# Kernel tuning notes

Measured on AMD Instinct MI355X. Metric: run time of the kernel, lower is better.

## Reference

```python
import jax, jax.numpy as jnp
import numpy as np

B, NV, H, D = 8, 16, 192, 512
NH = 8
HD = D // NH
DFF = 2048
EPS = 1e-5


def _bn(x, g, b):
    # x: (N, T, C); BatchNorm1d over channel C using batch stats (train mode)
    mu = jnp.mean(x, axis=(0, 1))
    var = jnp.var(x, axis=(0, 1))
    return (x - mu) / jnp.sqrt(var + EPS) * g + b


def _ff(x, w1, b1, w2, b2):
    h = jax.nn.gelu(jnp.einsum('bnhd,fd->bnhf', x, w1) + b1, approximate=False)
    return jnp.einsum('bnhf,df->bnhd', h, w2) + b2


def setup_inputs() -> dict:
    key = jax.random.key(0)
    ks = jax.random.split(key, 20)
    s = 0.02
    return {
        'src': jax.random.normal(ks[0], (B, NV, H, D), jnp.float32),
        'qk_w': jax.random.normal(ks[1], (2 * D, D), jnp.float32) * s,
        'qk_b': jnp.zeros((2 * D,), jnp.float32),
        'v_w': jax.random.normal(ks[2], (D, D), jnp.float32) * s,
        'v_b': jnp.zeros((D,), jnp.float32),
        'alpha_p': jax.random.normal(ks[3], (HD, 1), jnp.float32) * 0.1,
        'g_pre1': jnp.ones((D,), jnp.float32),
        'b_pre1': jnp.zeros((D,), jnp.float32),
        'g_pre2': jnp.ones((D,), jnp.float32),
        'b_pre2': jnp.zeros((D,), jnp.float32),
        'ff1_w1': jax.random.normal(ks[4], (DFF, D), jnp.float32) * s,
        'ff1_b1': jnp.zeros((DFF,), jnp.float32),
        'ff1_w2': jax.random.normal(ks[5], (D, DFF), jnp.float32) * s,
        'ff1_b2': jnp.zeros((D,), jnp.float32),
        'ff2_w1': jax.random.normal(ks[6], (DFF, D), jnp.float32) * s,
        'ff2_b1': jnp.zeros((DFF,), jnp.float32),
        'ff2_w2': jax.random.normal(ks[7], (D, DFF), jnp.float32) * s,
        'ff2_b2': jnp.zeros((D,), jnp.float32),
        'g_attn': jnp.ones((D,), jnp.float32),
        'b_attn': jnp.zeros((D,), jnp.float32),
    }


def reference(src, qk_w, qk_b, v_w, v_b, alpha_p,
              g_pre1, b_pre1, g_pre2, b_pre2,
              ff1_w1, ff1_b1, ff1_w2, ff1_b2,
              ff2_w1, ff2_b1, ff2_w2, ff2_b2,
              g_attn, b_attn):
    b, n, h, c = src.shape
    hd = c // NH
    # normalized input for q,k; raw for v
    src1 = src / jnp.linalg.norm(src, axis=-1, keepdims=True)
    qk = (jnp.einsum('bnhc,ec->bnhe', src1, qk_w) + qk_b)
    qk = qk.reshape(b, n, h, 2, NH, hd).transpose(3, 0, 1, 4, 2, 5)  # (2,b,n,NH,h,hd)
    q, k = qk[0], qk[1]
    v = (jnp.einsum('bnhc,ec->bnhe', src, v_w) + v_b)
    v = v.reshape(b, n, h, NH, hd).transpose(0, 1, 3, 2, 4)  # (b,n,NH,h,hd)

    # exponential-decay weights in FFT domain (branch: h != 7)
    a = jax.nn.sigmoid(alpha_p)                  # (hd,1)
    ar = jnp.arange(h - 1, -1, -1, dtype=src.dtype)
    weights = a * (1.0 - a) ** ar                # (hd, h)
    n2 = 2 * h
    w_f = jnp.fft.rfft(weights, n=n2, axis=-1)   # (hd, h+1)
    q_f = jnp.swapaxes(jnp.fft.rfft(q, n=n2, axis=-2), -1, -2) * w_f
    k_f = jnp.swapaxes(jnp.fft.rfft(k, n=n2, axis=-2), -1, -2) * w_f
    q1 = jnp.swapaxes(jnp.fft.irfft(q_f, n=n2, axis=-1)[..., :h], -1, -2)
    k1 = jnp.swapaxes(jnp.fft.irfft(k_f, n=n2, axis=-1)[..., :h], -1, -2)

    # token-axis attention (note: original divides by head_dim**-0.5 == * sqrt(hd))
    score_t = jnp.einsum('bnhed,bnhfd->bnhef', q1, k1) * (hd ** 0.5)
    attn_t = jax.nn.softmax(score_t, axis=-1)
    out_tok = jnp.einsum('bnhef,bnhfd->bnhed', attn_t, v)  # (b,n,NH,h,hd)
    o3 = _bn(out_tok.reshape(b * n, h, NH * hd), g_pre2, b_pre2).reshape(b, n, h, c)

    # hidden-axis attention on un-decayed q,k (scale = sqrt(h))
    score_h = jnp.einsum('bnhae,bnhaf->bnhef', q, k) * (h ** 0.5)
    attn_h = jax.nn.softmax(score_h, axis=-1)
    out_hid = jnp.einsum('bnhef,bnhaf->bnhae', attn_h, v)  # (b,n,NH,h,hd)
    o2 = _bn(out_hid.reshape(b * n, h, NH * hd), g_pre1, b_pre1).reshape(b, n, h, c)

    src2 = _ff(o3, ff1_w1, ff1_b1, ff1_w2, ff1_b2) + _ff(o2, ff2_w1, ff2_b1, ff2_w2, ff2_b2)
    out = src + src2
    out = _bn(out.reshape(b * n, h, c), g_attn, b_attn).reshape(b, n, h, c)
    return out
```

## Files before the change

kernel.cpp:

```cpp
#include <hip/hip_runtime.h>
#include <math.h>

#define SEQ 192
#define NTOK 24576
#define EPS 1e-5f

typedef __bf16 bf16x8 __attribute__((ext_vector_type(8)));
typedef __bf16 bf16x4 __attribute__((ext_vector_type(4)));
typedef float  f32x4  __attribute__((ext_vector_type(4)));

__device__ __forceinline__ void load_lds16(const __bf16* g, __bf16* l) {
    __builtin_amdgcn_global_load_lds(
        (const __attribute__((address_space(1))) uint32_t*)g,
        (__attribute__((address_space(3))) uint32_t*)l, 16, 0, 0);
}

__device__ __forceinline__ float gelu_f(float x) {
    float z = 1.5957691216057308f * x * fmaf(0.044715f, x*x, 1.f);
    float e = __expf(-z);
    return x * __builtin_amdgcn_rcpf(1.f + e);
}

__global__ __launch_bounds__(256) void cvtprep_k(
    const float* __restrict__ s0, const float* __restrict__ s1, const float* __restrict__ s2,
    const float* __restrict__ s3, const float* __restrict__ s4, const float* __restrict__ s5,
    __bf16* __restrict__ dst,
    const float* __restrict__ src, __bf16* __restrict__ srcb, __bf16* __restrict__ srcnb)
{
    if (blockIdx.x < 4864) {
        int i = blockIdx.x * 256 + threadIdx.x;
        int f = i * 4;
        const float* s; int off;
        if      (f <  524288) { s = s0; off = 0;       }
        else if (f <  786432) { s = s1; off = 524288;  }
        else if (f < 1835008) { s = s2; off = 786432;  }
        else if (f < 2883584) { s = s3; off = 1835008; }
        else if (f < 3932160) { s = s4; off = 2883584; }
        else                  { s = s5; off = 3932160; }
        f32x4 v = *(const f32x4*)&s[f - off];
        bf16x4 o;
        o[0]=(__bf16)v[0]; o[1]=(__bf16)v[1]; o[2]=(__bf16)v[2]; o[3]=(__bf16)v[3];
        ((bf16x4*)dst)[i] = o;
    } else {
        int blk = blockIdx.x - 4864;
        int w = threadIdx.x >> 6, lane = threadIdx.x & 63;
        size_t token = blk * 4 + w;
        const float* p = src + token * 512 + lane * 8;
        f32x4 a0 = *(const f32x4*)p;
        f32x4 a1 = *(const f32x4*)(p + 4);
        float s = a0[0]*a0[0]+a0[1]*a0[1]+a0[2]*a0[2]+a0[3]*a0[3]
                + a1[0]*a1[0]+a1[1]*a1[1]+a1[2]*a1[2]+a1[3]*a1[3];
#pragma unroll
        for (int off = 32; off; off >>= 1) s += __shfl_xor(s, off);
        float rs = rsqrtf(s);
        bf16x8 vb, vn;
#pragma unroll
        for (int q = 0; q < 4; q++) {
            vb[q]   = (__bf16)a0[q];      vn[q]   = (__bf16)(a0[q]*rs);
            vb[q+4] = (__bf16)a1[q];      vn[q+4] = (__bf16)(a1[q]*rs);
        }
        *(bf16x8*)&srcb[token*512 + lane*8]  = vb;
        *(bf16x8*)&srcnb[token*512 + lane*8] = vn;
    }
}

template<bool GELU, bool DUALM, bool NSPLIT>
__global__ __launch_bounds__(256) void gemm_k(
    const __bf16* __restrict__ A, const __bf16* __restrict__ B, __bf16* __restrict__ C,
    int N, int K, const float* __restrict__ bias,
    const __bf16* __restrict__ A2, const __bf16* __restrict__ B2, __bf16* __restrict__ C2,
    const float* __restrict__ bias2, int M1, int N2)
{
    __shared__ __bf16 As[8192];
    __shared__ __bf16 Bs[8192];
    const int tid = threadIdx.x, lane = tid & 63, w = tid >> 6;
    const int wr = w >> 1, wc = w & 1;
    const int b = blockIdx.y * gridDim.x + blockIdx.x;
    const int xcd = b & 7, bi = b >> 3;
    const int ypx = gridDim.y >> 3;
    int m0 = (xcd * ypx + bi / gridDim.x) * 128;
    int n0 = (bi % gridDim.x) * 128;
    if (DUALM && m0 >= M1)  { A = A2; B = B2; C = C2; bias = bias2; m0 -= M1; }
    if (NSPLIT && n0 >= M1) { A = A2; B = B2; C = C2; bias = bias2; n0 -= M1; N = N2; }
    const int fr = lane & 15, fq = lane >> 4;
    const int grow = 8*w + (lane >> 3);
    const int gcol = ((lane & 7) ^ (lane >> 3)) * 8;
    const __bf16* gB = B + (size_t)(n0 + grow) * K + gcol;
    const __bf16* gA = A + (size_t)(m0 + grow) * K + gcol;
    __bf16* ldsA = As + 8*w*64 + lane*8;
    __bf16* ldsB = Bs + 8*w*64 + lane*8;

    f32x4 acc[4][4];
#pragma unroll
    for (int i = 0; i < 4; i++)
#pragma unroll
        for (int j = 0; j < 4; j++) acc[i][j] = (f32x4){0.f,0.f,0.f,0.f};

    for (int k0 = 0; k0 < K; k0 += 64) {
#pragma unroll
        for (int i = 0; i < 4; i++)
            load_lds16(gA + k0 + (size_t)(32*i)*K, ldsA + i*2048);
#pragma unroll
        for (int i = 0; i < 4; i++)
            load_lds16(gB + k0 + (size_t)(32*i)*K, ldsB + i*2048);
        __syncthreads();
#pragma unroll
        for (int kk = 0; kk < 2; kk++) {
            bf16x8 af[4], bfv[4];
#pragma unroll
            for (int i = 0; i < 4; i++)
                af[i] = *(bf16x8*)&As[(wr*64 + i*16 + fr)*64 + (((kk*4+fq) ^ (fr&7))*8)];
#pragma unroll
            for (int j = 0; j < 4; j++)
                bfv[j] = *(bf16x8*)&Bs[(wc*64 + j*16 + fr)*64 + (((kk*4+fq) ^ (fr&7))*8)];
#pragma unroll
            for (int i = 0; i < 4; i++)
#pragma unroll
                for (int j = 0; j < 4; j++)
                    acc[i][j] = __builtin_amdgcn_mfma_f32_16x16x32_bf16(af[i], bfv[j], acc[i][j], 0, 0, 0);
        }
        __syncthreads();
    }
    const int r4 = lane >> 4, cc = lane & 15;
#pragma unroll
    for (int i = 0; i < 4; i++) {
#pragma unroll
        for (int r = 0; r < 4; r++) {
            int m = m0 + wr*64 + i*16 + r4*4 + r;
#pragma unroll
            for (int j = 0; j < 4; j++) {
                int n = n0 + wc*64 + j*16 + cc;
                float v = acc[i][j][r] + bias[n];
                if (GELU) v = gelu_f(v);
                C[(size_t)m * N + n] = (__bf16)v;
            }
        }
    }
}

__global__ __launch_bounds__(256) void w1scale_k(
    __bf16* __restrict__ w1a, __bf16* __restrict__ w1b, const float* __restrict__ coef01,
    const float* __restrict__ b1in, const float* __restrict__ b2in,
    float* __restrict__ b1out, float* __restrict__ b2out)
{
    const int half = blockIdx.x >> 9;
    __bf16* wbase = half ? w1b : w1a;
    const float* coef = coef01 + half*1024;
    const float* bin  = half ? b2in  : b1in;
    float* bout       = half ? b2out : b1out;
    const int wv = threadIdx.x >> 6, lane = threadIdx.x & 63;
    const int n = (blockIdx.x & 511) * 4 + wv;
    __bf16* p = wbase + (size_t)n * 512 + lane * 8;
    bf16x8 v = *(bf16x8*)p;
    f32x4 sc0 = *(const f32x4*)(coef + lane*8);
    f32x4 sc1 = *(const f32x4*)(coef + lane*8 + 4);
    f32x4 sh0 = *(const f32x4*)(coef + 512 + lane*8);
    f32x4 sh1 = *(const f32x4*)(coef + 512 + lane*8 + 4);
    float dot = 0.f;
    bf16x8 o;
#pragma unroll
    for (int q = 0; q < 4; q++) {
        float w0 = (float)v[q], w1 = (float)v[q+4];
        o[q]   = (__bf16)(w0 * sc0[q]);
        o[q+4] = (__bf16)(w1 * sc1[q]);
        dot = fmaf(w0, sh0[q], dot);
        dot = fmaf(w1, sh1[q], dot);
    }
    *(bf16x8*)p = o;
#pragma unroll
    for (int off = 32; off; off >>= 1) dot += __shfl_xor(dot, off);
    if (lane == 0) bout[n] = bin[n] + dot;
}

__global__ __launch_bounds__(256) void gemm2_k(
    const __bf16* __restrict__ A1, const __bf16* __restrict__ A2,
    const __bf16* __restrict__ B1, const __bf16* __restrict__ B2,
    float* __restrict__ C, const float* __restrict__ b1, const float* __restrict__ b2,
    const float* __restrict__ resid, float* __restrict__ st)
{
    __shared__ __bf16 As[2][4096];
    __shared__ __bf16 Bs[2][8192];
    const int tid = threadIdx.x, lane = tid & 63, w = tid >> 6;
    const int wr = w >> 1, wc = w & 1;
    const int vb = blockIdx.x;
    const int xcd = vb & 7, k2 = vb >> 3;
    const int m0 = (xcd*24 + (k2 >> 2)) * 64;
    const int n0 = (k2 & 3) * 128;
    const int fr = lane & 15, fq = lane >> 4;
    const int grow = 8*w + (lane >> 3);
    const int gcol = ((lane & 7) ^ (lane >> 3)) * 8;
    const int K = 2048;
    const int ldsoff = 8*w*64 + lane*8;
    const __bf16* gA1 = A1 + (size_t)(m0 + grow) * K + gcol;
    const __bf16* gA2 = A2 + (size_t)(m0 + grow) * K + gcol;
    const __bf16* gB1 = B1 + (size_t)(n0 + grow) * K + gcol;
    const __bf16* gB2 = B2 + (size_t)(n0 + grow) * K + gcol;

#define G2_STAGE(pb, it_) do {                                              \
        int half_ = (it_) >> 5, k0_ = ((it_) & 31) * 64;                    \
        const __bf16* ga_ = (half_ ? gA2 : gA1) + k0_;                      \
        const __bf16* gb_ = (half_ ? gB2 : gB1) + k0_;                      \
        load_lds16(ga_,                  &As[pb][ldsoff]);                  \
        load_lds16(ga_ + (size_t)32*K,   &As[pb][ldsoff + 2048]);           \
        load_lds16(gb_,                  &Bs[pb][ldsoff]);                  \
        load_lds16(gb_ + (size_t)32*K,   &Bs[pb][ldsoff + 2048]);           \
        load_lds16(gb_ + (size_t)64*K,   &Bs[pb][ldsoff + 4096]);           \
        load_lds16(gb_ + (size_t)96*K,   &Bs[pb][ldsoff + 6144]);           \
    } while (0)

    f32x4 acc[2][4];
#pragma unroll
    for (int i = 0; i < 2; i++)
#pragma unroll
        for (int j = 0; j < 4; j++) acc[i][j] = (f32x4){0.f,0.f,0.f,0.f};

    G2_STAGE(0, 0);
    asm volatile("s_waitcnt vmcnt(0)" ::: "memory");
    __syncthreads();
    for (int it = 0; it < 64; ++it) {
        const int cur = it & 1;
        if (it + 1 < 64) G2_STAGE(cur ^ 1, it + 1);
#pragma unroll
        for (int kk = 0; kk < 2; kk++) {
            bf16x8 af[2], bfv[4];
#pragma unroll
            for (int i = 0; i < 2; i++)
                af[i] = *(bf16x8*)&As[cur][(wr*32 + i*16 + fr)*64 + (((kk*4+fq) ^ (fr&7))*8)];
#pragma unroll
            for (int j = 0; j < 4; j++)
                bfv[j] = *(bf16x8*)&Bs[cur][(wc*64 + j*16 + fr)*64 + (((kk*4+fq) ^ (fr&7))*8)];
#pragma unroll
            for (int i = 0; i < 2; i++)
#pragma unroll
                for (int j = 0; j < 4; j++)
                    acc[i][j] = __builtin_amdgcn_mfma_f32_16x16x32_bf16(af[i], bfv[j], acc[i][j], 0, 0, 0);
        }
        asm volatile("s_waitcnt vmcnt(0)" ::: "memory");
        __syncthreads();
    }
#undef G2_STAGE

    const int r4 = lane >> 4, cc = lane & 15;
    float cs[4] = {0,0,0,0}, cq[4] = {0,0,0,0};
#pragma unroll
    for (int i = 0; i < 2; i++) {
#pragma unroll
        for (int r = 0; r < 4; r++) {
            int m = m0 + wr*32 + i*16 + r4*4 + r;
#pragma unroll
            for (int j = 0; j < 4; j++) {
                int n = n0 + wc*64 + j*16 + cc;
                size_t idx = (size_t)m * 512 + n;
                float v = acc[i][j][r] + b1[n] + b2[n] + resid[idx];
                C[idx] = v;
                cs[j] += v; cq[j] = fmaf(v, v, cq[j]);
            }
        }
    }
#pragma unroll
    for (int j = 0; j < 4; j++) {
        cs[j] += __shfl_xor(cs[j], 16); cs[j] += __shfl_xor(cs[j], 32);
        cq[j] += __shfl_xor(cq[j], 16); cq[j] += __shfl_xor(cq[j], 32);
    }
    if (r4 == 0) {
#pragma unroll
        for (int j = 0; j < 4; j++) {
            int n = n0 + wc*64 + j*16 + cc;
            atomicAdd(&st[n], cs[j]);
            atomicAdd(&st[512 + n], cq[j]);
        }
    }
}

__device__ __forceinline__ void hidden_attn_body(
    const __bf16* __restrict__ QKb, const __bf16* __restrict__ Vb, __bf16* __restrict__ OHb,
    __bf16* smem, int bn, int nh)
{
    __bf16* Qt = smem;
    __bf16* Kt = smem + 12800;
    __bf16* Ps = smem;
    __bf16* Vs = smem + 4608;
    const int tid = threadIdx.x, lane = tid & 63, w = tid >> 6;
    const int fr = lane & 15, fq = lane >> 4;
    const size_t rowbase = (size_t)bn * SEQ;

#pragma unroll
    for (int it = 0; it < 12; it++) {
        int tk = tid + (it % 6) * 256;
        int j = tk & 63, tg = tk >> 6;
        const __bf16* gsrc = QKb + (rowbase + tg*8)*1024 + nh*64 + j + (it >= 6 ? 512 : 0);
        bf16x8 v;
#pragma unroll
        for (int u = 0; u < 8; u++) v[u] = gsrc[(size_t)u*1024];
        __bf16* dst = (it >= 6 ? Kt : Qt) + j*200 + tg*8;
        *(bf16x8*)dst = v;
    }
    bf16x8 vreg[6];
#pragma unroll
    for (int it = 0; it < 6; it++) {
        int i = tid + it*256;
        int t = i >> 3, s = i & 7;
        vreg[it] = *(const bf16x8*)&Vb[(rowbase+t)*512 + nh*64 + s*8];
    }
    __syncthreads();

    f32x4 acc[4];
#pragma unroll
    for (int i = 0; i < 4; i++) acc[i] = (f32x4){0.f,0.f,0.f,0.f};
#pragma unroll
    for (int kc = 0; kc < 6; kc++) {
        bf16x8 a = *(bf16x8*)&Qt[(w*16 + fr)*200 + kc*32 + fq*8];
#pragma unroll
        for (int nt = 0; nt < 4; nt++) {
            bf16x8 b = *(bf16x8*)&Kt[(nt*16 + fr)*200 + kc*32 + fq*8];
            acc[nt] = __builtin_amdgcn_mfma_f32_16x16x32_bf16(a, b, acc[nt], 0, 0, 0);
        }
    }
    const float sc = 13.856406460551018f;
    float pn[4][4];
#pragma unroll
    for (int reg = 0; reg < 4; reg++) {
        float m = -1e30f;
#pragma unroll
        for (int nt = 0; nt < 4; nt++) { acc[nt][reg] *= sc; m = fmaxf(m, acc[nt][reg]); }
#pragma unroll
        for (int off = 1; off < 16; off <<= 1) m = fmaxf(m, __shfl_xor(m, off));
        float l = 0.f;
#pragma unroll
        for (int nt = 0; nt < 4; nt++) { pn[nt][reg] = __expf(acc[nt][reg] - m); l += pn[nt][reg]; }
#pragma unroll
        for (int off = 1; off < 16; off <<= 1) l += __shfl_xor(l, off);
        float inv = 1.f / l;
#pragma unroll
        for (int nt = 0; nt < 4; nt++) pn[nt][reg] *= inv;
    }
    __syncthreads();
#pragma unroll
    for (int nt = 0; nt < 4; nt++)
#pragma unroll
        for (int reg = 0; reg < 4; reg++)
            Ps[(w*16 + fq*4 + reg)*72 + nt*16 + fr] = (__bf16)pn[nt][reg];
#pragma unroll
    for (int it = 0; it < 6; it++) {
        int i = tid + it*256;
        int t = i >> 3, s = i & 7;
        *(bf16x8*)&Vs[t*72 + s*8] = vreg[it];
    }
    __syncthreads();

    f32x4 o[3][4];
#pragma unroll
    for (int i = 0; i < 3; i++)
#pragma unroll
        for (int j = 0; j < 4; j++) o[i][j] = (f32x4){0.f,0.f,0.f,0.f};
#pragma unroll
    for (int kc = 0; kc < 2; kc++) {
        bf16x8 av[3];
#pragma unroll
        for (int mt = 0; mt < 3; mt++)
            av[mt] = *(bf16x8*)&Vs[(48*w + mt*16 + fr)*72 + kc*32 + fq*8];
#pragma unroll
        for (int nt = 0; nt < 4; nt++) {
            bf16x8 b = *(bf16x8*)&Ps[(nt*16 + fr)*72 + kc*32 + fq*8];
#pragma unroll
            for (int mt = 0; mt < 3; mt++)
                o[mt][nt] = __builtin_amdgcn_mfma_f32_16x16x32_bf16(av[mt], b, o[mt][nt], 0, 0, 0);
        }
    }
    __bf16* obase = OHb + ((size_t)(bn*8 + nh)) * SEQ * 64;
#pragma unroll
    for (int mt = 0; mt < 3; mt++)
#pragma unroll
        for (int reg = 0; reg < 4; reg++) {
            int t = 48*w + mt*16 + fq*4 + reg;
#pragma unroll
            for (int nt = 0; nt < 4; nt++)
                obase[(size_t)t*64 + nt*16 + fr] = (__bf16)o[mt][nt][reg];
        }
}

__device__ __forceinline__ void token_attn_body(
    const __bf16* __restrict__ QKb, const __bf16* __restrict__ Vb, __bf16* __restrict__ OT,
    const float* __restrict__ alpha, __bf16* smem, int bn, int nh)
{
    __bf16* Qs = smem;
    __bf16* Ks = smem + 13824;
    __bf16* Vt = smem;
    __bf16* Pw = smem + 12800;
    const int tid = threadIdx.x, lane = tid & 63, w = tid >> 6;
    const int fr = lane & 15, fq = lane >> 4;
    const size_t rowbase = (size_t)bn * SEQ;

    for (int i = tid; i < 1536; i += 256) {
        int t = i >> 3, s = i & 7;
        const __bf16* g = QKb + (rowbase + t)*1024 + nh*64;
        *(bf16x8*)&Qs[t*72 + s*8] = *(const bf16x8*)&g[s*8];
        *(bf16x8*)&Ks[t*72 + s*8] = *(const bf16x8*)&g[512 + s*8];
    }
    bf16x8 vreg[6];
#pragma unroll
    for (int it = 0; it < 6; it++) {
        int tk = tid + it * 256;
        int d = tk & 63, tg = tk >> 6;
        const __bf16* gsrc = Vb + (rowbase + tg*8)*512 + nh*64 + d;
#pragma unroll
        for (int u = 0; u < 8; u++) vreg[it][u] = gsrc[(size_t)u*512];
    }
    __syncthreads();

    if (tid < 128) {
        const int d = tid & 63;
        __bf16* col = (tid < 64) ? (Qs + d) : (Ks + d);
        const float av = 1.f / (1.f + __expf(-alpha[d]));
        const float r = 1.f - av;
        float P = 0.f, pw = 1.f;
#pragma unroll 4
        for (int t = 0; t < SEQ; t++) {
            P = fmaf(pw, (float)col[t*72], P);
            col[t*72] = (__bf16)P;
            pw *= r;
        }
        float f = av;
#pragma unroll 4
        for (int t = SEQ-1; t >= 0; t--) {
            col[t*72] = (__bf16)((float)col[t*72] * f);
            f *= r;
        }
    }
    __syncthreads();

    f32x4 S[3][12];
#pragma unroll
    for (int i = 0; i < 3; i++)
#pragma unroll
        for (int j = 0; j < 12; j++) S[i][j] = (f32x4){0.f,0.f,0.f,0.f};
#pragma unroll
    for (int kc = 0; kc < 2; kc++) {
        bf16x8 aq[3];
#pragma unroll
        for (int mt = 0; mt < 3; mt++)
            aq[mt] = *(bf16x8*)&Qs[(48*w + mt*16 + fr)*72 + kc*32 + fq*8];
#pragma unroll
        for (int nt = 0; nt < 12; nt++) {
            bf16x8 b = *(bf16x8*)&Ks[(nt*16 + fr)*72 + kc*32 + fq*8];
#pragma unroll
            for (int mt = 0; mt < 3; mt++)
                S[mt][nt] = __builtin_amdgcn_mfma_f32_16x16x32_bf16(aq[mt], b, S[mt][nt], 0, 0, 0);
        }
    }
#pragma unroll
    for (int mt = 0; mt < 3; mt++)
#pragma unroll
        for (int reg = 0; reg < 4; reg++) {
            float m = -1e30f;
#pragma unroll
            for (int nt = 0; nt < 12; nt++) { S[mt][nt][reg] *= 8.f; m = fmaxf(m, S[mt][nt][reg]); }
#pragma unroll
            for (int off = 1; off < 16; off <<= 1) m = fmaxf(m, __shfl_xor(m, off));
            float l = 0.f;
#pragma unroll
            for (int nt = 0; nt < 12; nt++) { S[mt][nt][reg] = __expf(S[mt][nt][reg] - m); l += S[mt][nt][reg]; }
#pragma unroll
            for (int off = 1; off < 16; off <<= 1) l += __shfl_xor(l, off);
            float inv = 1.f / l;
#pragma unroll
            for (int nt = 0; nt < 12; nt++) S[mt][nt][reg] *= inv;
        }
    __syncthreads();
#pragma unroll
    for (int it = 0; it < 6; it++) {
        int tk = tid + it * 256;
        int d = tk & 63, tg = tk >> 6;
        *(bf16x8*)&Vt[d*200 + tg*8] = vreg[it];
    }
    __syncthreads();

    f32x4 O[3][4];
#pragma unroll
    for (int i = 0; i < 3; i++)
#pragma unroll
        for (int j = 0; j < 4; j++) O[i][j] = (f32x4){0.f,0.f,0.f,0.f};
    __bf16* myP = Pw + w*3456;
#pragma unroll
    for (int fc = 0; fc < 3; fc++) {
#pragma unroll
        for (int mt = 0; mt < 3; mt++)
#pragma unroll
            for (int j = 0; j < 4; j++)
#pragma unroll
                for (int reg = 0; reg < 4; reg++)
                    myP[(mt*16 + fq*4 + reg)*72 + j*16 + fr] = (__bf16)S[mt][fc*4 + j][reg];
#pragma unroll
        for (int kc = 0; kc < 2; kc++) {
            bf16x8 ap[3];
#pragma unroll
            for (int mt = 0; mt < 3; mt++)
                ap[mt] = *(bf16x8*)&myP[(mt*16 + fr)*72 + kc*32 + fq*8];
#pragma unroll
            for (int dt = 0; dt < 4; dt++) {
                bf16x8 b = *(bf16x8*)&Vt[(dt*16 + fr)*200 + fc*64 + kc*32 + fq*8];
#pragma unroll
                for (int mt = 0; mt < 3; mt++)
                    O[mt][dt] = __builtin_amdgcn_mfma_f32_16x16x32_bf16(ap[mt], b, O[mt][dt], 0, 0, 0);
            }
        }
    }
    __bf16* obase = OT + ((size_t)(bn*8 + nh)) * SEQ * 64;
#pragma unroll
    for (int mt = 0; mt < 3; mt++)
#pragma unroll
        for (int reg = 0; reg < 4; reg++) {
            int e = 48*w + mt*16 + fq*4 + reg;
#pragma unroll
            for (int dt = 0; dt < 4; dt++)
                obase[(size_t)e*64 + dt*16 + fr] = (__bf16)O[mt][dt][reg];
        }
}

__global__ __launch_bounds__(256) void attn_both_k(
    const __bf16* __restrict__ QKb, const __bf16* __restrict__ Vb,
    __bf16* __restrict__ OHb, __bf16* __restrict__ OT, const float* __restrict__ alpha)
{
    __shared__ __bf16 smem[27648];
    const int b = blockIdx.x;
    const int type = (b >> 8) & 1;
    const int idx = (b >> 9) * 256 + (b & 255);
    const int bn = idx >> 3, nh = idx & 7;
    if (type == 0) hidden_attn_body(QKb, Vb, OHb, smem, bn, nh);
    else           token_attn_body(QKb, Vb, OT, alpha, smem, bn, nh);
}

__global__ __launch_bounds__(256) void bn_stats1_k(const __bf16* __restrict__ x0,
    const __bf16* __restrict__ x1, float* __restrict__ part)
{
    __shared__ float red[3072];
    const __bf16* x = (blockIdx.x < 256) ? x0 : x1;
    const int blk = blockIdx.x & 255;
    const int col8 = threadIdx.x & 63;
    const int rl   = threadIdx.x >> 6;
    const size_t r0 = (size_t)blk * 96;
    f32x4 sA = {0,0,0,0}, sB = {0,0,0,0}, qA = {0,0,0,0}, qB = {0,0,0,0};
    for (int r = rl; r < 96; r += 4) {
        bf16x8 v = *(const bf16x8*)&x[(r0 + r)*512 + col8*8];
        f32x4 lo = { (float)v[0], (float)v[1], (float)v[2], (float)v[3] };
        f32x4 hi = { (float)v[4], (float)v[5], (float)v[6], (float)v[7] };
        sA += lo; sB += hi;
        qA += lo*lo; qB += hi*hi;
    }
    if (rl > 0) {
        float* p = &red[(rl-1)*1024];
        *(f32x4*)&p[col8*8]       = sA;  *(f32x4*)&p[col8*8 + 4]       = sB;
        *(f32x4*)&p[512 + col8*8] = qA;  *(f32x4*)&p[512 + col8*8 + 4] = qB;
    }
    __syncthreads();
    if (rl == 0) {
#pragma unroll
        for (int k = 0; k < 3; k++) {
            float* p = &red[k*1024];
            sA += *(f32x4*)&p[col8*8];       sB += *(f32x4*)&p[col8*8 + 4];
            qA += *(f32x4*)&p[512 + col8*8]; qB += *(f32x4*)&p[512 + col8*8 + 4];
        }
        float* o = &part[(size_t)blockIdx.x * 1024];
        *(f32x4*)&o[col8*8]       = sA;  *(f32x4*)&o[col8*8 + 4]       = sB;
        *(f32x4*)&o[512 + col8*8] = qA;  *(f32x4*)&o[512 + col8*8 + 4] = qB;
    }
}

__global__ __launch_bounds__(256) void bn_stats2_k(const float* __restrict__ part, float* __restrict__ st)
{
    int c = blockIdx.x * 256 + threadIdx.x;
    int half = c >> 10, cc = c & 1023;
    const float* p = part + (size_t)half * 262144;
    float s0 = 0.f, s1 = 0.f, s2 = 0.f, s3 = 0.f;
    for (int b = 0; b < 256; b += 4) {
        s0 += p[(size_t)b*1024 + cc];
        s1 += p[(size_t)(b+1)*1024 + cc];
        s2 += p[(size_t)(b+2)*1024 + cc];
        s3 += p[(size_t)(b+3)*1024 + cc];
    }
    st[c] = (s0 + s1) + (s2 + s3);
}

__global__ void bn_coef_k(const float* __restrict__ st,
                          const float* __restrict__ gA, const float* __restrict__ bA,
                          const float* __restrict__ gB, const float* __restrict__ bB,
                          float* __restrict__ coef)
{
    int tidx = threadIdx.x;
    int half = tidx >> 9, c = tidx & 511;
    const float* sb = st + half*1024;
    const float* g = half ? gB : gA;
    const float* b = half ? bB : bA;
    float* co = coef + half*1024;
    float mean = sb[c] * (1.f/24576.f);
    float var  = sb[512+c] * (1.f/24576.f) - mean*mean;
    float sc = rsqrtf(var + EPS) * g[c];
    co[c] = sc;
    co[512 + c] = b[c] - mean * sc;
}

__global__ __launch_bounds__(256) void bn_apply4_k(const float* __restrict__ x, const float* __restrict__ st,
    const float* __restrict__ g, const float* __restrict__ b, float* __restrict__ out)
{
    size_t i = (size_t)blockIdx.x * 256 + threadIdx.x;
    int col4 = i & 127;
    f32x4 v = ((const f32x4*)x)[i];
    f32x4 sm = ((const f32x4*)st)[col4];
    f32x4 sq = ((const f32x4*)(st + 512))[col4];
    f32x4 o;
#pragma unroll
    for (int j = 0; j < 4; j++) {
        int c = col4*4 + j;
        float mean = sm[j] * (1.f/24576.f);
        float var  = sq[j] * (1.f/24576.f) - mean*mean;
        o[j] = (v[j] - mean) * rsqrtf(var + EPS) * g[c] + b[c];
    }
    ((f32x4*)out)[i] = o;
}

extern "C" void kernel_launch(void* const* d_in, const int* in_sizes, int n_in,
                              void* d_out, int out_size, void* d_ws, size_t ws_size,
                              hipStream_t stream)
{
    const float* src    = (const float*)d_in[0];
    const float* qk_w   = (const float*)d_in[1];
    const float* qk_b   = (const float*)d_in[2];
    const float* v_w    = (const float*)d_in[3];
    const float* v_b    = (const float*)d_in[4];
    const float* alpha  = (const float*)d_in[5];
    const float* g_pre1 = (const float*)d_in[6];
    const float* b_pre1 = (const float*)d_in[7];
    const float* g_pre2 = (const float*)d_in[8];
    const float* b_pre2 = (const float*)d_in[9];
    const float* ff1_w1 = (const float*)d_in[10];
    const float* ff1_b1 = (const float*)d_in[11];
    const float* ff1_w2 = (const float*)d_in[12];
    const float* ff1_b2 = (const float*)d_in[13];
    const float* ff2_w1 = (const float*)d_in[14];
    const float* ff2_b1 = (const float*)d_in[15];
    const float* ff2_w2 = (const float*)d_in[16];
    const float* ff2_b2 = (const float*)d_in[17];
    const float* g_attn = (const float*)d_in[18];
    const float* b_attn = (const float*)d_in[19];
    float* out = (float*)d_out;

    __bf16* wq   = (__bf16*)d_ws;
    __bf16* wv   = wq  + 524288;
    __bf16* w11  = wv  + 262144;
    __bf16* w12  = w11 + 1048576;
    __bf16* w21  = w12 + 1048576;
    __bf16* w22  = w21 + 1048576;
    __bf16* srcb  = w22 + 1048576;
    __bf16* srcnb = srcb + (size_t)NTOK*512;
    __bf16* QKb   = srcnb + (size_t)NTOK*512;
    __bf16* Vb    = QKb + (size_t)NTOK*1024;
    __bf16* OHbf  = Vb + (size_t)NTOK*512;
    __bf16* o3bf  = OHbf + (size_t)NTOK*512;
    float*  stats = (float*)(o3bf + (size_t)NTOK*512);
    float*  coef0 = stats + 3072;
    float*  part0 = coef0 + 2048;
    float*  bias1p = part0 + 2*262144;
    float*  bias2p = bias1p + 2048;
    __bf16* H1 = srcb;
    __bf16* H2 = H1 + (size_t)12288*2048;
    float *st2 = stats + 2048;

    hipMemsetAsync(st2, 0, 1024*sizeof(float), stream);

    cvtprep_k<<<4864 + NTOK/4, 256, 0, stream>>>(qk_w, v_w, ff1_w1, ff1_w2, ff2_w1, ff2_w2, wq,
                                                 src, srcb, srcnb);

    gemm_k<false,false,true><<<dim3(12, 192), 256, 0, stream>>>(
        srcnb, wq, QKb, 1024, 512, qk_b,
        srcb,  wv, Vb,  v_b, 1024, 512);

    attn_both_k<<<2048, 256, 0, stream>>>(QKb, Vb, OHbf, o3bf, alpha);

    bn_stats1_k<<<512, 256, 0, stream>>>(o3bf, OHbf, part0);
    bn_stats2_k<<<8, 256, 0, stream>>>(part0, stats);
    bn_coef_k<<<1, 1024, 0, stream>>>(stats, g_pre2, b_pre2, g_pre1, b_pre1, coef0);
    w1scale_k<<<1024, 256, 0, stream>>>(w11, w21, coef0, ff1_b1, ff2_b1, bias1p, bias2p);

    for (int ch = 0; ch < 2; ch++) {
        size_t off = (size_t)ch * 12288 * 512;
        gemm_k<true,true,false><<<dim3(16, 192), 256, 0, stream>>>(
            o3bf + off, w11, H1, 2048, 512, bias1p,
            OHbf + off, w21, H2, bias2p, 12288, 2048);
        gemm2_k<<<768, 256, 0, stream>>>(H1, H2, w12, w22, out + off,
                                         ff1_b2, ff2_b2, src + off, st2);
    }

    bn_apply4_k<<<12288, 256, 0, stream>>>(out, st2, g_attn, b_attn, out);
}
```

Before: 642.3 us.

## Fuse BatchNorm statistics into attention epilogue via LDS and global atomics

```diff
diff --git a/kernel.cpp b/kernel.cpp
--- a/kernel.cpp
+++ b/kernel.cpp
@@ -274,12 +274,13 @@
 
 __device__ __forceinline__ void hidden_attn_body(
     const __bf16* __restrict__ QKb, const __bf16* __restrict__ Vb, __bf16* __restrict__ OHb,
-    __bf16* smem, int bn, int nh)
+    float* __restrict__ stg, __bf16* smem, int bn, int nh)
 {
     __bf16* Qt = smem;
     __bf16* Kt = smem + 12800;
     __bf16* Ps = smem;
     __bf16* Vs = smem + 4608;
+    float* stLds = (float*)(smem + 27648);
     const int tid = threadIdx.x, lane = tid & 63, w = tid >> 6;
     const int fr = lane & 15, fq = lane >> 4;
     const size_t rowbase = (size_t)bn * SEQ;
@@ -346,6 +347,7 @@
         int t = i >> 3, s = i & 7;
         *(bf16x8*)&Vs[t*72 + s*8] = vreg[it];
     }
+    ((f32x4*)stLds)[tid] = (f32x4){0.f,0.f,0.f,0.f};
     __syncthreads();
 
     f32x4 o[3][4];
@@ -368,25 +370,56 @@
         }
     }
     __bf16* obase = OHb + ((size_t)(bn*8 + nh)) * SEQ * 64;
+    float cs[4][4], cq[4][4];
+#pragma unroll
+    for (int r = 0; r < 4; r++)
+#pragma unroll
+        for (int j = 0; j < 4; j++) { cs[r][j] = 0.f; cq[r][j] = 0.f; }
 #pragma unroll
     for (int mt = 0; mt < 3; mt++)
 #pragma unroll
         for (int reg = 0; reg < 4; reg++) {
             int t = 48*w + mt*16 + fq*4 + reg;
 #pragma unroll
-            for (int nt = 0; nt < 4; nt++)
-                obase[(size_t)t*64 + nt*16 + fr] = (__bf16)o[mt][nt][reg];
-        }
+            for (int nt = 0; nt < 4; nt++) {
+                __bf16 ob = (__bf16)o[mt][nt][reg];
+                obase[(size_t)t*64 + nt*16 + fr] = ob;
+                float vf = (float)ob;
+                cs[reg][nt] += vf; cq[reg][nt] = fmaf(vf, vf, cq[reg][nt]);
+            }
+        }
+#pragma unroll
+    for (int reg = 0; reg < 4; reg++)
+#pragma unroll
+        for (int nt = 0; nt < 4; nt++) {
+            cs[reg][nt] += __shfl_xor(cs[reg][nt], 32);
+            cq[reg][nt] += __shfl_xor(cq[reg][nt], 32);
+        }
+    if (fq < 2) {
+#pragma unroll
+        for (int reg = 0; reg < 4; reg++)
+#pragma unroll
+            for (int nt = 0; nt < 4; nt++) {
+                int c = ((fq*4 + reg) & 7)*64 + nt*16 + fr;
+                atomicAdd(&stLds[c], cs[reg][nt]);
+                atomicAdd(&stLds[512 + c], cq[reg][nt]);
+            }
+    }
+    __syncthreads();
+#pragma unroll
+    for (int j = 0; j < 4; j++)
+        atomicAdd(&stg[tid*4 + j], stLds[tid*4 + j]);
 }
 
 __device__ __forceinline__ void token_attn_body(
     const __bf16* __restrict__ QKb, const __bf16* __restrict__ Vb, __bf16* __restrict__ OT,
-    const float* __restrict__ alpha, __bf16* smem, int bn, int nh)
+    const float* __restrict__ alpha, float* __restrict__ stg, __bf16* smem, int bn, int nh)
 {
     __bf16* Qs = smem;
     __bf16* Ks = smem + 13824;
     __bf16* Vt = smem;
     __bf16* Pw = smem + 12800;
+    float* stLds = (float*)(smem + 27648);
     const int tid = threadIdx.x, lane = tid & 63, w = tid >> 6;
     const int fr = lane & 15, fq = lane >> 4;
     const size_t rowbase = (size_t)bn * SEQ;
@@ -414,17 +447,24 @@
         const float av = 1.f / (1.f + __expf(-alpha[d]));
         const float r = 1.f - av;
         float P = 0.f, pw = 1.f;
-#pragma unroll 4
-        for (int t = 0; t < SEQ; t++) {
-            P = fmaf(pw, (float)col[t*72], P);
-            col[t*72] = (__bf16)P;
-            pw *= r;
+        for (int t0 = 0; t0 < SEQ; t0 += 16) {
+            float x[16];
+#pragma unroll
+            for (int u = 0; u < 16; u++) x[u] = (float)col[(t0+u)*72];
+#pragma unroll
+            for (int u = 0; u < 16; u++) { P = fmaf(pw, x[u], P); x[u] = P; pw *= r; }
+#pragma unroll
+            for (int u = 0; u < 16; u++) col[(t0+u)*72] = (__bf16)x[u];
         }
         float f = av;
-#pragma unroll 4
-        for (int t = SEQ-1; t >= 0; t--) {
-            col[t*72] = (__bf16)((float)col[t*72] * f);
-            f *= r;
+        for (int t0 = SEQ-16; t0 >= 0; t0 -= 16) {
+            float x[16];
+#pragma unroll
+            for (int u = 0; u < 16; u++) x[u] = (float)col[(t0+u)*72];
+#pragma unroll
+            for (int u = 15; u >= 0; u--) { x[u] *= f; f *= r; }
+#pragma unroll
+            for (int u = 0; u < 16; u++) col[(t0+u)*72] = (__bf16)x[u];
         }
     }
     __syncthreads();
@@ -473,6 +513,7 @@
         int d = tk & 63, tg = tk >> 6;
         *(bf16x8*)&Vt[d*200 + tg*8] = vreg[it];
     }
+    ((f32x4*)stLds)[tid] = (f32x4){0.f,0.f,0.f,0.f};
     __syncthreads();
 
     f32x4 O[3][4];
@@ -506,79 +547,59 @@
         }
     }
     __bf16* obase = OT + ((size_t)(bn*8 + nh)) * SEQ * 64;
+    float cs[4][4], cq[4][4];
+#pragma unroll
+    for (int r = 0; r < 4; r++)
+#pragma unroll
+        for (int j = 0; j < 4; j++) { cs[r][j] = 0.f; cq[r][j] = 0.f; }
 #pragma unroll
     for (int mt = 0; mt < 3; mt++)
 #pragma unroll
         for (int reg = 0; reg < 4; reg++) {
             int e = 48*w + mt*16 + fq*4 + reg;
 #pragma unroll
-            for (int dt = 0; dt < 4; dt++)
-                obase[(size_t)e*64 + dt*16 + fr] = (__bf16)O[mt][dt][reg];
-        }
+            for (int dt = 0; dt < 4; dt++) {
+                __bf16 ob = (__bf16)O[mt][dt][reg];
+                obase[(size_t)e*64 + dt*16 + fr] = ob;
+                float vf = (float)ob;
+                cs[reg][dt] += vf; cq[reg][dt] = fmaf(vf, vf, cq[reg][dt]);
+            }
+        }
+#pragma unroll
+    for (int reg = 0; reg < 4; reg++)
+#pragma unroll
+        for (int dt = 0; dt < 4; dt++) {
+            cs[reg][dt] += __shfl_xor(cs[reg][dt], 32);
+            cq[reg][dt] += __shfl_xor(cq[reg][dt], 32);
+        }
+    if (fq < 2) {
+#pragma unroll
+        for (int reg = 0; reg < 4; reg++)
+#pragma unroll
+            for (int dt = 0; dt < 4; dt++) {
+                int c = ((fq*4 + reg) & 7)*64 + dt*16 + fr;
+                atomicAdd(&stLds[c], cs[reg][dt]);
+                atomicAdd(&stLds[512 + c], cq[reg][dt]);
+            }
+    }
+    __syncthreads();
+#pragma unroll
+    for (int j = 0; j < 4; j++)
+        atomicAdd(&stg[tid*4 + j], stLds[tid*4 + j]);
 }
 
 __global__ __launch_bounds__(256) void attn_both_k(
     const __bf16* __restrict__ QKb, const __bf16* __restrict__ Vb,
-    __bf16* __restrict__ OHb, __bf16* __restrict__ OT, const float* __restrict__ alpha)
-{
-    __shared__ __bf16 smem[27648];
+    __bf16* __restrict__ OHb, __bf16* __restrict__ OT, const float* __restrict__ alpha,
+    float* __restrict__ st)
+{
+    __shared__ __bf16 smem[29696];
     const int b = blockIdx.x;
     const int type = (b >> 8) & 1;
     const int idx = (b >> 9) * 256 + (b & 255);
     const int bn = idx >> 3, nh = idx & 7;
-    if (type == 0) hidden_attn_body(QKb, Vb, OHb, smem, bn, nh);
-    else           token_attn_body(QKb, Vb, OT, alpha, smem, bn, nh);
-}
-
-__global__ __launch_bounds__(256) void bn_stats1_k(const __bf16* __restrict__ x0,
-    const __bf16* __restrict__ x1, float* __restrict__ part)
-{
-    __shared__ float red[3072];
-    const __bf16* x = (blockIdx.x < 256) ? x0 : x1;
-    const int blk = blockIdx.x & 255;
-    const int col8 = threadIdx.x & 63;
-    const int rl   = threadIdx.x >> 6;
-    const size_t r0 = (size_t)blk * 96;
-    f32x4 sA = {0,0,0,0}, sB = {0,0,0,0}, qA = {0,0,0,0}, qB = {0,0,0,0};
-    for (int r = rl; r < 96; r += 4) {
-        bf16x8 v = *(const bf16x8*)&x[(r0 + r)*512 + col8*8];
-        f32x4 lo = { (float)v[0], (float)v[1], (float)v[2], (float)v[3] };
-        f32x4 hi = { (float)v[4], (float)v[5], (float)v[6], (float)v[7] };
-        sA += lo; sB += hi;
-        qA += lo*lo; qB += hi*hi;
-    }
-    if (rl > 0) {
-        float* p = &red[(rl-1)*1024];
-        *(f32x4*)&p[col8*8]       = sA;  *(f32x4*)&p[col8*8 + 4]       = sB;
-        *(f32x4*)&p[512 + col8*8] = qA;  *(f32x4*)&p[512 + col8*8 + 4] = qB;
-    }
-    __syncthreads();
-    if (rl == 0) {
-#pragma unroll
-        for (int k = 0; k < 3; k++) {
-            float* p = &red[k*1024];
-            sA += *(f32x4*)&p[col8*8];       sB += *(f32x4*)&p[col8*8 + 4];
-            qA += *(f32x4*)&p[512 + col8*8]; qB += *(f32x4*)&p[512 + col8*8 + 4];
-        }
-        float* o = &part[(size_t)blockIdx.x * 1024];
-        *(f32x4*)&o[col8*8]       = sA;  *(f32x4*)&o[col8*8 + 4]       = sB;
-        *(f32x4*)&o[512 + col8*8] = qA;  *(f32x4*)&o[512 + col8*8 + 4] = qB;
-    }
-}
-
-__global__ __launch_bounds__(256) void bn_stats2_k(const float* __restrict__ part, float* __restrict__ st)
-{
-    int c = blockIdx.x * 256 + threadIdx.x;
-    int half = c >> 10, cc = c & 1023;
-    const float* p = part + (size_t)half * 262144;
-    float s0 = 0.f, s1 = 0.f, s2 = 0.f, s3 = 0.f;
-    for (int b = 0; b < 256; b += 4) {
-        s0 += p[(size_t)b*1024 + cc];
-        s1 += p[(size_t)(b+1)*1024 + cc];
-        s2 += p[(size_t)(b+2)*1024 + cc];
-        s3 += p[(size_t)(b+3)*1024 + cc];
-    }
-    st[c] = (s0 + s1) + (s2 + s3);
+    if (type == 0) hidden_attn_body(QKb, Vb, OHb, st + 1024, smem, bn, nh);
+    else           token_attn_body(QKb, Vb, OT, alpha, st, smem, bn, nh);
 }
 
 __global__ void bn_coef_k(const float* __restrict__ st,
@@ -658,14 +679,13 @@
     __bf16* o3bf  = OHbf + (size_t)NTOK*512;
     float*  stats = (float*)(o3bf + (size_t)NTOK*512);
     float*  coef0 = stats + 3072;
-    float*  part0 = coef0 + 2048;
-    float*  bias1p = part0 + 2*262144;
+    float*  bias1p = coef0 + 2048;
     float*  bias2p = bias1p + 2048;
     __bf16* H1 = srcb;
     __bf16* H2 = H1 + (size_t)12288*2048;
     float *st2 = stats + 2048;
 
-    hipMemsetAsync(st2, 0, 1024*sizeof(float), stream);
+    hipMemsetAsync(stats, 0, 3072*sizeof(float), stream);
 
     cvtprep_k<<<4864 + NTOK/4, 256, 0, stream>>>(qk_w, v_w, ff1_w1, ff1_w2, ff2_w1, ff2_w2, wq,
                                                  src, srcb, srcnb);
@@ -674,10 +694,8 @@
         srcnb, wq, QKb, 1024, 512, qk_b,
         srcb,  wv, Vb,  v_b, 1024, 512);
 
-    attn_both_k<<<2048, 256, 0, stream>>>(QKb, Vb, OHbf, o3bf, alpha);
-
-    bn_stats1_k<<<512, 256, 0, stream>>>(o3bf, OHbf, part0);
-    bn_stats2_k<<<8, 256, 0, stream>>>(part0, stats);
+    attn_both_k<<<2048, 256, 0, stream>>>(QKb, Vb, OHbf, o3bf, alpha, stats);
+
     bn_coef_k<<<1, 1024, 0, stream>>>(stats, g_pre2, b_pre2, g_pre1, b_pre1, coef0);
     w1scale_k<<<1024, 256, 0, stream>>>(w11, w21, coef0, ff1_b1, ff2_b1, bias1p, bias2p);
 
```

Result: slower. 714.0 us (+11.2%).
